# Kernel optimization log

Measured on AMD Instinct MI355X. Metric: run time of the kernel, lower is better.

The kernel has to match this reference:

```python
import jax, jax.numpy as jnp
import numpy as np

E, D, DFF = 8, 1024, 4096

def setup_inputs() -> dict:
    key = jax.random.key(0)
    ks = jax.random.split(key, 10)
    s = 0.02
    return {
        "x":  jax.random.normal(ks[0], (4, 2048, D), dtype=jnp.float32),
        "Wr": jax.random.normal(ks[1], (D, E), dtype=jnp.float32) * s,
        "br": jnp.zeros((E,), dtype=jnp.float32),
        "W1": jax.random.normal(ks[2], (E, D, DFF), dtype=jnp.float32) * s,
        "b1": jnp.zeros((E, DFF), dtype=jnp.float32),
        "W2": jax.random.normal(ks[3], (E, D, DFF), dtype=jnp.float32) * s,
        "b2": jnp.zeros((E, DFF), dtype=jnp.float32),
        "W3": jax.random.normal(ks[4], (E, DFF, D), dtype=jnp.float32) * s,
        "b3": jnp.zeros((E, D), dtype=jnp.float32),
    }

def reference(x, Wr, br, W1, b1, W2, b2, W3, b3):
    b, s, d = x.shape
    xt = x.reshape(b * s, d)                       # [T, D]
    logits = xt @ Wr + br                          # [T, E]
    pr, idx = jax.lax.top_k(logits, 2)             # [T, 2]
    w = jax.nn.softmax(pr, axis=-1)                # softmax over the 2 selected experts
    # combine weight per (token, expert): sum of routing weights where expert selected
    onehot = jax.nn.one_hot(idx, W1.shape[0], dtype=x.dtype)  # [T, 2, E]
    cw = jnp.einsum('tk,tke->te', w, onehot)       # [T, E]
    y = jnp.zeros_like(xt)
    for e in range(W1.shape[0]):                   # small fixed expert loop
        h = jax.nn.silu(xt @ W1[e] + b1[e]) * (xt @ W2[e] + b2[e])  # SwiGLU [T, DFF]
        y = y + (h @ W3[e] + b3[e]) * cw[:, e:e + 1]
    return y.reshape(b, s, d)
```

## Files before the change

### kernel.cpp

```cpp
#include <hip/hip_runtime.h>

#define T_TOK 8192
#define DIM   1024
#define DFF_  4096
#define NE    8
#define MAXT  144

typedef float  f32x4 __attribute__((ext_vector_type(4)));
typedef __bf16 b16x8 __attribute__((ext_vector_type(8)));

__device__ __forceinline__ unsigned short f2bf(float f) {
  union { float f; unsigned int u; } v; v.f = f;
  unsigned int r = v.u + 0x7fffu + ((v.u >> 16) & 1u);
  return (unsigned short)(r >> 16);
}

__device__ __forceinline__ void gload_lds16(const void* g, void* l) {
  __builtin_amdgcn_global_load_lds((const __attribute__((address_space(1))) void*)g,
                                   (__attribute__((address_space(3))) void*)l,
                                   16, 0, 0);
}

#define DRAIN_VMCNT() asm volatile("s_waitcnt vmcnt(0)" ::: "memory")

__global__ __launch_bounds__(256) void transpose_cvt(const float* __restrict__ src,
                                                     unsigned short* __restrict__ dst,
                                                     int R, int C) {
  __shared__ float tile[64][65];
  size_t mat = (size_t)blockIdx.z * R * C;
  int c0 = blockIdx.x * 64, r0 = blockIdx.y * 64;
  int lc = threadIdx.x & 63, q = threadIdx.x >> 6;
  const float* s = src + mat + (size_t)r0 * C + c0;
#pragma unroll
  for (int i = 0; i < 16; i++) {
    int r = q + i * 4;
    tile[r][lc] = s[(size_t)r * C + lc];
  }
  __syncthreads();
  unsigned short* d = dst + mat + (size_t)c0 * R + r0;
#pragma unroll
  for (int i = 0; i < 16; i++) {
    int cc = q + i * 4;
    d[(size_t)cc * R + lc] = f2bf(tile[lc][cc]);
  }
}

__global__ __launch_bounds__(256) void router_k(const float* __restrict__ x,
                                                const float* __restrict__ Wr,
                                                const float* __restrict__ br,
                                                unsigned short* __restrict__ Xbf,
                                                int* __restrict__ top2e,
                                                float* __restrict__ top2w) {
  int wid = threadIdx.x >> 6, lane = threadIdx.x & 63;
  int t = blockIdx.x * 4 + wid;
  const float* xr = x + (size_t)t * DIM;
  unsigned short* xb = Xbf + (size_t)t * DIM;
  float s[NE];
#pragma unroll
  for (int e = 0; e < NE; e++) s[e] = 0.f;
  for (int i = 0; i < DIM / 64; i++) {
    int dd = i * 64 + lane;
    float xv = xr[dd];
    xb[dd] = f2bf(xv);
    const float* w = Wr + (size_t)dd * NE;
#pragma unroll
    for (int e = 0; e < NE; e++) s[e] += xv * w[e];
  }
#pragma unroll
  for (int m = 32; m >= 1; m >>= 1) {
#pragma unroll
    for (int e = 0; e < NE; e++) s[e] += __shfl_xor(s[e], m, 64);
  }
  if (lane == 0) {
#pragma unroll
    for (int e = 0; e < NE; e++) s[e] += br[e];
    int e0 = 0;
#pragma unroll
    for (int e = 1; e < NE; e++) if (s[e] > s[e0]) e0 = e;
    int e1 = (e0 == 0) ? 1 : 0;
#pragma unroll
    for (int e = 0; e < NE; e++) if (e != e0 && s[e] > s[e1]) e1 = e;
    float w0 = 1.f / (1.f + expf(s[e1] - s[e0]));
    top2e[2 * t] = e0; top2e[2 * t + 1] = e1;
    top2w[2 * t] = w0; top2w[2 * t + 1] = 1.f - w0;
  }
}

__global__ __launch_bounds__(256) void count_k(const int* __restrict__ top2e,
                                               int* __restrict__ counts) {
  __shared__ int lcnt[NE];
  if (threadIdx.x < NE) lcnt[threadIdx.x] = 0;
  __syncthreads();
  int t = blockIdx.x * 256 + threadIdx.x;
  atomicAdd(&lcnt[top2e[2 * t]], 1);
  atomicAdd(&lcnt[top2e[2 * t + 1]], 1);
  __syncthreads();
  if (threadIdx.x < NE) atomicAdd(&counts[threadIdx.x], lcnt[threadIdx.x]);
}

__global__ void scan_build(int* __restrict__ ctrl) {
  if (threadIdx.x != 0 || blockIdx.x != 0) return;
  int* counts = ctrl;
  int* offsets = ctrl + 8;
  int* cursors = ctrl + 16;
  int* ntile = ctrl + 24;
  int* tileE = ctrl + 32;
  int* tileM = ctrl + 32 + MAXT;
  int o = 0;
  for (int e = 0; e < NE; e++) { offsets[e] = o; cursors[e] = o; o += counts[e]; }
  int nt = 0;
  for (int e = 0; e < NE; e++)
    for (int m0 = 0; m0 < counts[e]; m0 += 128) { tileE[nt] = e; tileM[nt] = m0; nt++; }
  ntile[0] = nt;
}

__global__ __launch_bounds__(256) void scatter_k(const int* __restrict__ top2e,
                                                 const float* __restrict__ top2w,
                                                 int* __restrict__ cursors,
                                                 int* __restrict__ list_tok,
                                                 float* __restrict__ list_w) {
  __shared__ int lcnt[NE];
  __shared__ int lbase[NE];
  int tid = threadIdx.x;
  if (tid < NE) lcnt[tid] = 0;
  __syncthreads();
  int t = blockIdx.x * 256 + tid;
  int e0 = top2e[2 * t], e1 = top2e[2 * t + 1];
  int r0 = atomicAdd(&lcnt[e0], 1);
  int r1 = atomicAdd(&lcnt[e1], 1);
  __syncthreads();
  if (tid < NE) lbase[tid] = atomicAdd(&cursors[tid], lcnt[tid]);
  __syncthreads();
  int p0 = lbase[e0] + r0, p1 = lbase[e1] + r1;
  list_tok[p0] = t; list_w[p0] = top2w[2 * t];
  list_tok[p1] = t; list_w[p1] = top2w[2 * t + 1];
}

__global__ __launch_bounds__(512) void gemm1_k(const unsigned short* __restrict__ Xbf,
                                               const unsigned short* __restrict__ W1T,
                                               const unsigned short* __restrict__ W2T,
                                               const float* __restrict__ b1,
                                               const float* __restrict__ b2,
                                               unsigned short* __restrict__ H,
                                               const int* __restrict__ list_tok,
                                               const int* __restrict__ ctrl) {
  const int* counts = ctrl; const int* offsets = ctrl + 8;
  const int* ntile = ctrl + 24;
  const int* tileE = ctrl + 32; const int* tileM = ctrl + 32 + MAXT;
  int bt = blockIdx.y;
  if (bt >= ntile[0]) return;
  int e = tileE[bt], m0 = tileM[bt];
  int Me = counts[e], off = offsets[e];
  int n0 = blockIdx.x * 128;

  __shared__ unsigned short lds[2][3 * 128 * 32];

  int tid = threadIdx.x, lane = tid & 63, wid = tid >> 6;
  int wr = wid >> 2, wc = wid & 3;

  const unsigned short* gsrc[3];
  unsigned ldsoff[3];
  {
    int lr = lane >> 2;
    int sc = ((lane & 3) ^ ((lane >> 3) & 3)) * 8;
#pragma unroll
    for (int j = 0; j < 3; j++) {
      int c = wid * 3 + j;
      ldsoff[j] = c * 512;
      if (c < 8) {
        int r = c * 16 + lr;
        int tok = (m0 + r < Me) ? list_tok[off + m0 + r] : list_tok[off];
        gsrc[j] = Xbf + (size_t)tok * DIM + sc;
      } else if (c < 16) {
        int n = n0 + (c - 8) * 16 + lr;
        gsrc[j] = W1T + ((size_t)e * DFF_ + n) * DIM + sc;
      } else {
        int n = n0 + (c - 16) * 16 + lr;
        gsrc[j] = W2T + ((size_t)e * DFF_ + n) * DIM + sc;
      }
    }
  }

  f32x4 acc1[4][2], acc2[4][2];
#pragma unroll
  for (int i = 0; i < 4; i++)
#pragma unroll
    for (int j = 0; j < 2; j++) {
      acc1[i][j] = f32x4{0.f, 0.f, 0.f, 0.f};
      acc2[i][j] = f32x4{0.f, 0.f, 0.f, 0.f};
    }

#pragma unroll
  for (int j = 0; j < 3; j++) gload_lds16(gsrc[j], (void*)(&lds[0][ldsoff[j]]));
  DRAIN_VMCNT();
  __syncthreads();

  int cur = 0;
  const int NK = DIM / 32;
  for (int kt = 0; kt < NK; kt++) {
    if (kt + 1 < NK) {
#pragma unroll
      for (int j = 0; j < 3; j++)
        gload_lds16(gsrc[j] + (kt + 1) * 32, (void*)(&lds[cur ^ 1][ldsoff[j]]));
    }
    const unsigned short* sA  = &lds[cur][0];
    const unsigned short* sB1 = sA + 4096;
    const unsigned short* sB2 = sA + 8192;
    int colg = lane >> 4;
    b16x8 aF[4], bF1[2], bF2[2];
#pragma unroll
    for (int fi = 0; fi < 4; fi++) {
      int row = wr * 64 + fi * 16 + (lane & 15);
      aF[fi] = *(const b16x8*)(sA + row * 32 + ((colg ^ ((row >> 1) & 3)) * 8));
    }
#pragma unroll
    for (int fj = 0; fj < 2; fj++) {
      int row = wc * 32 + fj * 16 + (lane & 15);
      int sw = (colg ^ ((row >> 1) & 3)) * 8;
      bF1[fj] = *(const b16x8*)(sB1 + row * 32 + sw);
      bF2[fj] = *(const b16x8*)(sB2 + row * 32 + sw);
    }
#pragma unroll
    for (int fi = 0; fi < 4; fi++)
#pragma unroll
      for (int fj = 0; fj < 2; fj++) {
        acc1[fi][fj] = __builtin_amdgcn_mfma_f32_16x16x32_bf16(aF[fi], bF1[fj], acc1[fi][fj], 0, 0, 0);
        acc2[fi][fj] = __builtin_amdgcn_mfma_f32_16x16x32_bf16(aF[fi], bF2[fj], acc2[fi][fj], 0, 0, 0);
      }
    DRAIN_VMCNT();
    __syncthreads();
    cur ^= 1;
  }

#pragma unroll
  for (int fi = 0; fi < 4; fi++)
#pragma unroll
    for (int fj = 0; fj < 2; fj++) {
      int col = n0 + wc * 32 + fj * 16 + (lane & 15);
      float bb1 = b1[e * DFF_ + col], bb2 = b2[e * DFF_ + col];
      int rbase = wr * 64 + fi * 16 + (lane >> 4) * 4;
#pragma unroll
      for (int r = 0; r < 4; r++) {
        int rr = rbase + r;
        if (m0 + rr < Me) {
          float c1 = acc1[fi][fj][r] + bb1;
          float c2 = acc2[fi][fj][r] + bb2;
          float h = c1 * c2 / (1.f + __expf(-c1));
          H[(size_t)(off + m0 + rr) * DFF_ + col] = f2bf(h);
        }
      }
    }
}

__global__ __launch_bounds__(512) void gemm2_k(const unsigned short* __restrict__ H,
                                               const unsigned short* __restrict__ W3T,
                                               const float* __restrict__ b3,
                                               const int* __restrict__ list_tok,
                                               const float* __restrict__ list_w,
                                               float* __restrict__ y,
                                               const int* __restrict__ ctrl) {
  const int* counts = ctrl; const int* offsets = ctrl + 8;
  const int* ntile = ctrl + 24;
  const int* tileE = ctrl + 32; const int* tileM = ctrl + 32 + MAXT;
  int bt = blockIdx.y;
  if (bt >= ntile[0]) return;
  int e = tileE[bt], m0 = tileM[bt];
  int Me = counts[e], off = offsets[e];
  int n0 = blockIdx.x * 128;

  __shared__ unsigned short lds[2][2 * 128 * 64];

  int tid = threadIdx.x, lane = tid & 63, wid = tid >> 6;
  int wr = wid >> 2, wc = wid & 3;

  const unsigned short* gsrc[4];
  unsigned ldsoff[4];
  {
    int lr = lane >> 3;
    int sc = ((lane & 7) ^ (lane >> 3)) * 8;
#pragma unroll
    for (int j = 0; j < 4; j++) {
      int c = wid * 4 + j;
      ldsoff[j] = c * 512;
      if (c < 16) {
        int r = c * 8 + lr;
        int pos = (m0 + r < Me) ? (off + m0 + r) : off;
        gsrc[j] = H + (size_t)pos * DFF_ + sc;
      } else {
        int n = n0 + (c - 16) * 8 + lr;
        gsrc[j] = W3T + ((size_t)e * DIM + n) * DFF_ + sc;
      }
    }
  }

  f32x4 acc[4][2];
#pragma unroll
  for (int i = 0; i < 4; i++)
#pragma unroll
    for (int j = 0; j < 2; j++) acc[i][j] = f32x4{0.f, 0.f, 0.f, 0.f};

#pragma unroll
  for (int j = 0; j < 4; j++) gload_lds16(gsrc[j], (void*)(&lds[0][ldsoff[j]]));
  DRAIN_VMCNT();
  __syncthreads();

  int cur = 0;
  const int NK = DFF_ / 64;
  for (int kt = 0; kt < NK; kt++) {
    if (kt + 1 < NK) {
#pragma unroll
      for (int j = 0; j < 4; j++)
        gload_lds16(gsrc[j] + (kt + 1) * 64, (void*)(&lds[cur ^ 1][ldsoff[j]]));
    }
    const unsigned short* sA = &lds[cur][0];
    const unsigned short* sB = sA + 128 * 64;
    int colg = lane >> 4;
#pragma unroll
    for (int kk = 0; kk < 2; kk++) {
      b16x8 aF[4], bF[2];
#pragma unroll
      for (int fi = 0; fi < 4; fi++) {
        int row = wr * 64 + fi * 16 + (lane & 15);
        aF[fi] = *(const b16x8*)(sA + row * 64 + (((kk * 4 + colg) ^ (row & 7)) * 8));
      }
#pragma unroll
      for (int fj = 0; fj < 2; fj++) {
        int row = wc * 32 + fj * 16 + (lane & 15);
        bF[fj] = *(const b16x8*)(sB + row * 64 + (((kk * 4 + colg) ^ (row & 7)) * 8));
      }
#pragma unroll
      for (int fi = 0; fi < 4; fi++)
#pragma unroll
        for (int fj = 0; fj < 2; fj++)
          acc[fi][fj] = __builtin_amdgcn_mfma_f32_16x16x32_bf16(aF[fi], bF[fj], acc[fi][fj], 0, 0, 0);
    }
    DRAIN_VMCNT();
    __syncthreads();
    cur ^= 1;
  }

#pragma unroll
  for (int fi = 0; fi < 4; fi++)
#pragma unroll
    for (int fj = 0; fj < 2; fj++) {
      int col = n0 + wc * 32 + fj * 16 + (lane & 15);
      float bb3 = b3[e * DIM + col];
      int rbase = wr * 64 + fi * 16 + (lane >> 4) * 4;
#pragma unroll
      for (int r = 0; r < 4; r++) {
        int rr = rbase + r;
        if (m0 + rr < Me) {
          int pos = off + m0 + rr;
          float v = list_w[pos] * (acc[fi][fj][r] + bb3);
          atomicAdd(&y[(size_t)list_tok[pos] * DIM + col], v);
        }
      }
    }
}

extern "C" void kernel_launch(void* const* d_in, const int* in_sizes, int n_in,
                              void* d_out, int out_size, void* d_ws, size_t ws_size,
                              hipStream_t stream) {
  (void)in_sizes; (void)n_in; (void)ws_size;
  const float* x  = (const float*)d_in[0];
  const float* Wr = (const float*)d_in[1];
  const float* br = (const float*)d_in[2];
  const float* W1 = (const float*)d_in[3];
  const float* b1 = (const float*)d_in[4];
  const float* W2 = (const float*)d_in[5];
  const float* b2 = (const float*)d_in[6];
  const float* W3 = (const float*)d_in[7];
  const float* b3 = (const float*)d_in[8];
  float* y = (float*)d_out;
  char* ws = (char*)d_ws;

  const size_t matB = (size_t)NE * DFF_ * DIM * 2;
  size_t oW1T = 0;
  size_t oW2T = oW1T + matB;
  size_t oXbf = oW2T + matB;
  size_t oH   = oXbf + (size_t)T_TOK * DIM * 2;
  size_t oT2e = oH + (size_t)2 * T_TOK * DFF_ * 2;
  size_t oT2w = oT2e + (size_t)2 * T_TOK * 4;
  size_t oLtk = oT2w + (size_t)2 * T_TOK * 4;
  size_t oLw  = oLtk + (size_t)2 * T_TOK * 4;
  size_t oCtl = oLw + (size_t)2 * T_TOK * 4;

  unsigned short* W1T = (unsigned short*)(ws + oW1T);
  unsigned short* W2T = (unsigned short*)(ws + oW2T);
  unsigned short* W3T = (unsigned short*)(ws + oW1T);
  unsigned short* Xbf = (unsigned short*)(ws + oXbf);
  unsigned short* Hb  = (unsigned short*)(ws + oH);
  int*   top2e = (int*)(ws + oT2e);
  float* top2w = (float*)(ws + oT2w);
  int*   ltok  = (int*)(ws + oLtk);
  float* lw    = (float*)(ws + oLw);
  int*   ctrl  = (int*)(ws + oCtl);

  hipMemsetAsync(y, 0, (size_t)out_size * 4, stream);
  hipMemsetAsync(ctrl, 0, (32 + 2 * MAXT) * 4, stream);

  transpose_cvt<<<dim3(DFF_ / 64, DIM / 64, NE), 256, 0, stream>>>(W1, W1T, DIM, DFF_);
  transpose_cvt<<<dim3(DFF_ / 64, DIM / 64, NE), 256, 0, stream>>>(W2, W2T, DIM, DFF_);
  router_k<<<dim3(T_TOK / 4), 256, 0, stream>>>(x, Wr, br, Xbf, top2e, top2w);
  count_k<<<dim3(T_TOK / 256), 256, 0, stream>>>(top2e, ctrl);
  scan_build<<<dim3(1), 64, 0, stream>>>(ctrl);
  scatter_k<<<dim3(T_TOK / 256), 256, 0, stream>>>(top2e, top2w, ctrl + 16, ltok, lw);
  gemm1_k<<<dim3(DFF_ / 128, MAXT - 8), 512, 0, stream>>>(Xbf, W1T, W2T, b1, b2, Hb, ltok, ctrl);
  transpose_cvt<<<dim3(DIM / 64, DFF_ / 64, NE), 256, 0, stream>>>(W3, W3T, DFF_, DIM);
  gemm2_k<<<dim3(DIM / 128, MAXT - 8), 512, 0, stream>>>(Hb, W3T, b3, ltok, lw, y, ctrl);
}
```

Baseline: 764.6 us.

## Fuse expert counting into router, widen transpose stores, hoist LDS offsets

The transpose kernel now packs two bf16 values into each 32-bit store, halving the number of narrow global writes. Expert counting moves into the router kernel through shared-memory atomics, which removes the separate count_k launch and its re-read of top2e. Both GEMM kernels compute their swizzled LDS fragment offsets once before the k-loop instead of on every iteration. The offset hoisting keeps a few more registers live, and the transpose write pattern changes from one row per wave to paired rows.

```diff
diff --git a/kernel.cpp b/kernel.cpp
--- a/kernel.cpp
+++ b/kernel.cpp
@@ -38,10 +38,13 @@
   }
   __syncthreads();
   unsigned short* d = dst + mat + (size_t)c0 * R + r0;
-#pragma unroll
-  for (int i = 0; i < 16; i++) {
-    int cc = q + i * 4;
-    d[(size_t)cc * R + lc] = f2bf(tile[lc][cc]);
+  int lc2 = (threadIdx.x & 31) * 2, cq = threadIdx.x >> 5;
+#pragma unroll
+  for (int i = 0; i < 8; i++) {
+    int cc = cq + i * 8;
+    unsigned lo = f2bf(tile[lc2][cc]);
+    unsigned hi = f2bf(tile[lc2 + 1][cc]);
+    *(unsigned*)(&d[(size_t)cc * R + lc2]) = lo | (hi << 16);
   }
 }
 
@@ -50,7 +53,11 @@
                                                 const float* __restrict__ br,
                                                 unsigned short* __restrict__ Xbf,
                                                 int* __restrict__ top2e,
-                                                float* __restrict__ top2w) {
+                                                float* __restrict__ top2w,
+                                                int* __restrict__ counts) {
+  __shared__ int lcnt[NE];
+  if (threadIdx.x < NE) lcnt[threadIdx.x] = 0;
+  __syncthreads();
   int wid = threadIdx.x >> 6, lane = threadIdx.x & 63;
   int t = blockIdx.x * 4 + wid;
   const float* xr = x + (size_t)t * DIM;
@@ -83,17 +90,9 @@
     float w0 = 1.f / (1.f + expf(s[e1] - s[e0]));
     top2e[2 * t] = e0; top2e[2 * t + 1] = e1;
     top2w[2 * t] = w0; top2w[2 * t + 1] = 1.f - w0;
-  }
-}
-
-__global__ __launch_bounds__(256) void count_k(const int* __restrict__ top2e,
-                                               int* __restrict__ counts) {
-  __shared__ int lcnt[NE];
-  if (threadIdx.x < NE) lcnt[threadIdx.x] = 0;
-  __syncthreads();
-  int t = blockIdx.x * 256 + threadIdx.x;
-  atomicAdd(&lcnt[top2e[2 * t]], 1);
-  atomicAdd(&lcnt[top2e[2 * t + 1]], 1);
+    atomicAdd(&lcnt[e0], 1);
+    atomicAdd(&lcnt[e1], 1);
+  }
   __syncthreads();
   if (threadIdx.x < NE) atomicAdd(&counts[threadIdx.x], lcnt[threadIdx.x]);
 }
@@ -181,6 +180,21 @@
     }
   }
 
+  unsigned aoff[4], boff[2];
+  {
+    int colg = lane >> 4;
+#pragma unroll
+    for (int fi = 0; fi < 4; fi++) {
+      int row = wr * 64 + fi * 16 + (lane & 15);
+      aoff[fi] = row * 32 + ((colg ^ ((row >> 1) & 3)) * 8);
+    }
+#pragma unroll
+    for (int fj = 0; fj < 2; fj++) {
+      int row = wc * 32 + fj * 16 + (lane & 15);
+      boff[fj] = row * 32 + ((colg ^ ((row >> 1) & 3)) * 8);
+    }
+  }
+
   f32x4 acc1[4][2], acc2[4][2];
 #pragma unroll
   for (int i = 0; i < 4; i++)
@@ -189,6 +203,27 @@
       acc1[i][j] = f32x4{0.f, 0.f, 0.f, 0.f};
       acc2[i][j] = f32x4{0.f, 0.f, 0.f, 0.f};
     }
+
+  auto compute = [&](const unsigned short* base) {
+    const unsigned short* sA  = base;
+    const unsigned short* sB1 = base + 4096;
+    const unsigned short* sB2 = base + 8192;
+    b16x8 aF[4], bF1[2], bF2[2];
+#pragma unroll
+    for (int fi = 0; fi < 4; fi++) aF[fi] = *(const b16x8*)(sA + aoff[fi]);
+#pragma unroll
+    for (int fj = 0; fj < 2; fj++) {
+      bF1[fj] = *(const b16x8*)(sB1 + boff[fj]);
+      bF2[fj] = *(const b16x8*)(sB2 + boff[fj]);
+    }
+#pragma unroll
+    for (int fi = 0; fi < 4; fi++)
+#pragma unroll
+      for (int fj = 0; fj < 2; fj++) {
+        acc1[fi][fj] = __builtin_amdgcn_mfma_f32_16x16x32_bf16(aF[fi], bF1[fj], acc1[fi][fj], 0, 0, 0);
+        acc2[fi][fj] = __builtin_amdgcn_mfma_f32_16x16x32_bf16(aF[fi], bF2[fj], acc2[fi][fj], 0, 0, 0);
+      }
+  };
 
 #pragma unroll
   for (int j = 0; j < 3; j++) gload_lds16(gsrc[j], (void*)(&lds[0][ldsoff[j]]));
@@ -203,30 +238,7 @@
       for (int j = 0; j < 3; j++)
         gload_lds16(gsrc[j] + (kt + 1) * 32, (void*)(&lds[cur ^ 1][ldsoff[j]]));
     }
-    const unsigned short* sA  = &lds[cur][0];
-    const unsigned short* sB1 = sA + 4096;
-    const unsigned short* sB2 = sA + 8192;
-    int colg = lane >> 4;
-    b16x8 aF[4], bF1[2], bF2[2];
-#pragma unroll
-    for (int fi = 0; fi < 4; fi++) {
-      int row = wr * 64 + fi * 16 + (lane & 15);
-      aF[fi] = *(const b16x8*)(sA + row * 32 + ((colg ^ ((row >> 1) & 3)) * 8));
-    }
-#pragma unroll
-    for (int fj = 0; fj < 2; fj++) {
-      int row = wc * 32 + fj * 16 + (lane & 15);
-      int sw = (colg ^ ((row >> 1) & 3)) * 8;
-      bF1[fj] = *(const b16x8*)(sB1 + row * 32 + sw);
-      bF2[fj] = *(const b16x8*)(sB2 + row * 32 + sw);
-    }
-#pragma unroll
-    for (int fi = 0; fi < 4; fi++)
-#pragma unroll
-      for (int fj = 0; fj < 2; fj++) {
-        acc1[fi][fj] = __builtin_amdgcn_mfma_f32_16x16x32_bf16(aF[fi], bF1[fj], acc1[fi][fj], 0, 0, 0);
-        acc2[fi][fj] = __builtin_amdgcn_mfma_f32_16x16x32_bf16(aF[fi], bF2[fj], acc2[fi][fj], 0, 0, 0);
-      }
+    compute(&lds[cur][0]);
     DRAIN_VMCNT();
     __syncthreads();
     cur ^= 1;
@@ -293,11 +305,47 @@
     }
   }
 
+  unsigned aoff[2][4], boff[2][2];
+  {
+    int colg = lane >> 4;
+#pragma unroll
+    for (int kk = 0; kk < 2; kk++) {
+#pragma unroll
+      for (int fi = 0; fi < 4; fi++) {
+        int row = wr * 64 + fi * 16 + (lane & 15);
+        aoff[kk][fi] = row * 64 + (((kk * 4 + colg) ^ (row & 7)) * 8);
+      }
+#pragma unroll
+      for (int fj = 0; fj < 2; fj++) {
+        int row = wc * 32 + fj * 16 + (lane & 15);
+        boff[kk][fj] = row * 64 + (((kk * 4 + colg) ^ (row & 7)) * 8);
+      }
+    }
+  }
+
   f32x4 acc[4][2];
 #pragma unroll
   for (int i = 0; i < 4; i++)
 #pragma unroll
     for (int j = 0; j < 2; j++) acc[i][j] = f32x4{0.f, 0.f, 0.f, 0.f};
+
+  auto compute = [&](const unsigned short* base) {
+    const unsigned short* sA = base;
+    const unsigned short* sB = base + 128 * 64;
+#pragma unroll
+    for (int kk = 0; kk < 2; kk++) {
+      b16x8 aF[4], bF[2];
+#pragma unroll
+      for (int fi = 0; fi < 4; fi++) aF[fi] = *(const b16x8*)(sA + aoff[kk][fi]);
+#pragma unroll
+      for (int fj = 0; fj < 2; fj++) bF[fj] = *(const b16x8*)(sB + boff[kk][fj]);
+#pragma unroll
+      for (int fi = 0; fi < 4; fi++)
+#pragma unroll
+        for (int fj = 0; fj < 2; fj++)
+          acc[fi][fj] = __builtin_amdgcn_mfma_f32_16x16x32_bf16(aF[fi], bF[fj], acc[fi][fj], 0, 0, 0);
+    }
+  };
 
 #pragma unroll
   for (int j = 0; j < 4; j++) gload_lds16(gsrc[j], (void*)(&lds[0][ldsoff[j]]));
@@ -312,28 +360,7 @@
       for (int j = 0; j < 4; j++)
         gload_lds16(gsrc[j] + (kt + 1) * 64, (void*)(&lds[cur ^ 1][ldsoff[j]]));
     }
-    const unsigned short* sA = &lds[cur][0];
-    const unsigned short* sB = sA + 128 * 64;
-    int colg = lane >> 4;
-#pragma unroll
-    for (int kk = 0; kk < 2; kk++) {
-      b16x8 aF[4], bF[2];
-#pragma unroll
-      for (int fi = 0; fi < 4; fi++) {
-        int row = wr * 64 + fi * 16 + (lane & 15);
-        aF[fi] = *(const b16x8*)(sA + row * 64 + (((kk * 4 + colg) ^ (row & 7)) * 8));
-      }
-#pragma unroll
-      for (int fj = 0; fj < 2; fj++) {
-        int row = wc * 32 + fj * 16 + (lane & 15);
-        bF[fj] = *(const b16x8*)(sB + row * 64 + (((kk * 4 + colg) ^ (row & 7)) * 8));
-      }
-#pragma unroll
-      for (int fi = 0; fi < 4; fi++)
-#pragma unroll
-        for (int fj = 0; fj < 2; fj++)
-          acc[fi][fj] = __builtin_amdgcn_mfma_f32_16x16x32_bf16(aF[fi], bF[fj], acc[fi][fj], 0, 0, 0);
-    }
+    compute(&lds[cur][0]);
     DRAIN_VMCNT();
     __syncthreads();
     cur ^= 1;
@@ -401,8 +428,7 @@
 
   transpose_cvt<<<dim3(DFF_ / 64, DIM / 64, NE), 256, 0, stream>>>(W1, W1T, DIM, DFF_);
   transpose_cvt<<<dim3(DFF_ / 64, DIM / 64, NE), 256, 0, stream>>>(W2, W2T, DIM, DFF_);
-  router_k<<<dim3(T_TOK / 4), 256, 0, stream>>>(x, Wr, br, Xbf, top2e, top2w);
-  count_k<<<dim3(T_TOK / 256), 256, 0, stream>>>(top2e, ctrl);
+  router_k<<<dim3(T_TOK / 4), 256, 0, stream>>>(x, Wr, br, Xbf, top2e, top2w, ctrl);
   scan_build<<<dim3(1), 64, 0, stream>>>(ctrl);
   scatter_k<<<dim3(T_TOK / 256), 256, 0, stream>>>(top2e, top2w, ctrl + 16, ltok, lw);
   gemm1_k<<<dim3(DFF_ / 128, MAXT - 8), 512, 0, stream>>>(Xbf, W1T, W2T, b1, b2, Hb, ltok, ctrl);
```

New measurement: 771.1 us. Within noise of the previous version (+0.9%).
